# Kernel tuning notes

Measured on AMD Instinct MI355X. Metric: run time of the kernel, lower is better.

Reference implementation:

```python
import jax, jax.numpy as jnp
import numpy as np

B, S, D = 4, 1024, 4096
HQ, HKV, HD = 32, 8, 128
N_REP = HQ // HKV


def _rope(x, cos, sin):
    # x: [b, s, h, hd]; cos/sin: [s, hd//2]; pairs are (x[..., 2i], x[..., 2i+1])
    xr = x[..., 0::2]
    xi = x[..., 1::2]
    c = cos[None, :, None, :]
    s = sin[None, :, None, :]
    out_r = xr * c - xi * s
    out_i = xr * s + xi * c
    return jnp.stack([out_r, out_i], axis=-1).reshape(x.shape)


def setup_inputs() -> dict:
    key = jax.random.key(0)
    ks = jax.random.split(key, 6)
    x = jax.random.normal(ks[0], (B, S, D), dtype=jnp.float32)
    wq = jax.random.normal(ks[1], (HQ * HD, D), dtype=jnp.float32) * 0.02
    wk = jax.random.normal(ks[2], (HKV * HD, D), dtype=jnp.float32) * 0.02
    wv = jax.random.normal(ks[3], (HKV * HD, D), dtype=jnp.float32) * 0.02
    wo = jax.random.normal(ks[4], (D, HQ * HD), dtype=jnp.float32) * 0.02
    # standard rotary frequencies, theta=10000
    inv_freq = 1.0 / (10000.0 ** (np.arange(0, HD, 2, dtype=np.float32) / HD))
    angles = np.outer(np.arange(S, dtype=np.float32), inv_freq)  # [S, HD//2]
    freqs_cos = jnp.asarray(np.cos(angles), dtype=jnp.float32)
    freqs_sin = jnp.asarray(np.sin(angles), dtype=jnp.float32)
    cache_k = jnp.zeros((B, S, HKV, HD), dtype=jnp.float32)
    cache_v = jnp.zeros((B, S, HKV, HD), dtype=jnp.float32)
    return {"x": x, "wq": wq, "wk": wk, "wv": wv, "wo": wo,
            "freqs_cos": freqs_cos, "freqs_sin": freqs_sin,
            "cache_k": cache_k, "cache_v": cache_v, "start_pos": 0}


def reference(x, wq, wk, wv, wo, freqs_cos, freqs_sin, cache_k, cache_v, start_pos):
    b, s, _ = x.shape
    xq = jnp.einsum('bsd,od->bso', x, wq).reshape(b, s, HQ, HD)
    xk = jnp.einsum('bsd,od->bso', x, wk).reshape(b, s, HKV, HD)
    xv = jnp.einsum('bsd,od->bso', x, wv).reshape(b, s, HKV, HD)
    xq = _rope(xq, freqs_cos, freqs_sin)
    xk = _rope(xk, freqs_cos, freqs_sin)
    # KV-cache append (intended semantics: store keys/values)
    cache_k = jax.lax.dynamic_update_slice(cache_k, xk, (0, start_pos, 0, 0))
    cache_v = jax.lax.dynamic_update_slice(cache_v, xv, (0, start_pos, 0, 0))
    keys = cache_k[:, :start_pos + s]      # [b, kv, HKV, HD]
    values = cache_v[:, :start_pos + s]
    # GQA repeat_kv -> [b, kv, HQ, HD]
    keys = jnp.repeat(keys, N_REP, axis=2)
    values = jnp.repeat(values, N_REP, axis=2)
    scores = jnp.einsum('bqhd,bkhd->bhqk', xq, keys) / jnp.sqrt(jnp.float32(HD))
    probs = jax.nn.softmax(scores.astype(jnp.float32), axis=-1).astype(xq.dtype)
    out = jnp.einsum('bhqk,bkhd->bqhd', probs, values).reshape(b, s, HQ * HD)
    return jnp.einsum('bso,do->bsd', out, wo)
```

## Files before the change

### kernel.cpp

```cpp
#include <hip/hip_runtime.h>

typedef __bf16 bf16_t;
typedef __bf16 bf16x8 __attribute__((ext_vector_type(8)));
typedef __bf16 bf16x4 __attribute__((ext_vector_type(4)));
typedef float  f32x4  __attribute__((ext_vector_type(4)));
typedef short  s16x4  __attribute__((ext_vector_type(4)));

#define SEQ    1024
#define DMODEL 4096
#define NHQ    32
#define NHKV   8
#define HDIM   128

#define GLOAD_LDS16(g, l)                                                  \
    __builtin_amdgcn_global_load_lds(                                      \
        (const __attribute__((address_space(1))) unsigned int*)(g),        \
        (__attribute__((address_space(3))) unsigned int*)(l), 16, 0, 0)

__global__ __launch_bounds__(256)
void f2b(const float* __restrict__ in, bf16_t* __restrict__ out, int n8)
{
    int i = blockIdx.x * 256 + threadIdx.x;
    if (i >= n8) return;
    const float4* p = (const float4*)in + 2 * (size_t)i;
    float4 a = p[0], b = p[1];
    bf16x8 o;
    o[0] = (bf16_t)a.x; o[1] = (bf16_t)a.y; o[2] = (bf16_t)a.z; o[3] = (bf16_t)a.w;
    o[4] = (bf16_t)b.x; o[5] = (bf16_t)b.y; o[6] = (bf16_t)b.z; o[7] = (bf16_t)b.w;
    *((bf16x8*)out + i) = o;
}

#define MFMA_(a, b, c) __builtin_amdgcn_mfma_f32_16x16x32_bf16(a, b, c, 0, 0, 0)
#define BAR    __builtin_amdgcn_s_barrier()
#define SCB    __builtin_amdgcn_sched_barrier(0)
#define PRIO1  __builtin_amdgcn_s_setprio(1)
#define PRIO0  __builtin_amdgcn_s_setprio(0)
#define WLG0   do { asm volatile("s_waitcnt lgkmcnt(0)" ::: "memory"); SCB; } while (0)
#define WLG8   do { asm volatile("s_waitcnt lgkmcnt(8)" ::: "memory"); SCB; } while (0)
#define WVM4   do { asm volatile("s_waitcnt vmcnt(4)" ::: "memory"); SCB; } while (0)

#define SA(bufo, half, ktb)  do {                                          \
    const char* g_ = ((half) ? aS1 : aS0) + (ktb);                         \
    GLOAD_LDS16(g_,      sd + (bufo) + (half) * 8192);                     \
    GLOAD_LDS16(g_ + 64, sd + (bufo) + (half) * 8192 + 16384);             \
} while (0)
#define SB(bufo, half, ktb)  do {                                          \
    const char* g_ = ((half) ? bS1 : bS0) + (ktb);                         \
    GLOAD_LDS16(g_,      sd + (bufo) + 32768 + (half) * 8192);             \
    GLOAD_LDS16(g_ + 64, sd + (bufo) + 32768 + (half) * 8192 + 16384);     \
} while (0)
#define LDA(bufo, mh) do { _Pragma("unroll")                               \
    for (int j = 0; j < 4; ++j) {                                          \
        afq[j][0] = *(const bf16x8*)(lds + (bufo) + aRow + (mh)*4096 + j*1024);         \
        afq[j][1] = *(const bf16x8*)(lds + (bufo) + aRow + (mh)*4096 + j*1024 + 16384); \
    } } while (0)
#define LDB(bufo, nh, dst) do { _Pragma("unroll")                          \
    for (int n2 = 0; n2 < 2; ++n2) {                                       \
        dst[n2][0] = *(const bf16x8*)(lds + (bufo) + bRow + (nh)*2048 + n2*1024);         \
        dst[n2][1] = *(const bf16x8*)(lds + (bufo) + bRow + (nh)*2048 + n2*1024 + 16384); \
    } } while (0)
#define MMQ(mlo, bfx, nlo) do { _Pragma("unroll")                          \
    for (int j = 0; j < 4; ++j) {                                          \
        acc[(mlo)+j][(nlo)  ] = MFMA_(afq[j][0], bfx[0][0], acc[(mlo)+j][(nlo)  ]); \
        acc[(mlo)+j][(nlo)  ] = MFMA_(afq[j][1], bfx[0][1], acc[(mlo)+j][(nlo)  ]); \
        acc[(mlo)+j][(nlo)+1] = MFMA_(afq[j][0], bfx[1][0], acc[(mlo)+j][(nlo)+1]); \
        acc[(mlo)+j][(nlo)+1] = MFMA_(afq[j][1], bfx[1][1], acc[(mlo)+j][(nlo)+1]); \
    } } while (0)

template<bool OUT_F32>
__global__ __launch_bounds__(512, 2)
void gemm256(const bf16_t* __restrict__ A, const bf16_t* __restrict__ B,
             void* __restrict__ Cv, int M, int N, int K, int nbn)
{
    __shared__ __align__(16) char lds[131072];

    const int nwg = gridDim.x;
    const int bid0 = blockIdx.x;
    const int bid = (bid0 & 7) * (nwg >> 3) + (bid0 >> 3);
    const int bm = bid / nbn, bn = bid % nbn;
    const int t = threadIdx.x;
    const int lane = t & 63, wid = t >> 6;
    const int wm = wid >> 2, wn = wid & 3;
    const int l15 = lane & 15, lg = lane >> 4;
    const int m0 = bm * 256, n0 = bn * 256;

    const int Krb = K * 2;
    const int srow = t >> 2;
    const int schunk = (((t & 3) ^ ((t >> 3) & 3)) << 4);
    const char* aS0 = (const char*)A + (size_t)(m0 + srow) * Krb + schunk;
    const char* aS1 = (const char*)A + (size_t)(m0 + 128 + srow) * Krb + schunk;
    const char* bS0 = (const char*)B + (size_t)(n0 + srow) * Krb + schunk;
    const char* bS1 = (const char*)B + (size_t)(n0 + 128 + srow) * Krb + schunk;
    char* sd = lds + t * 16;

    const int rchunk = ((lg ^ ((l15 >> 1) & 3)) << 4);
    const int aRow = (wm * 128 + l15) * 64 + rchunk;
    const int bRow = 32768 + (wn * 64 + l15) * 64 + rchunk;

    const int NT = K >> 6;
    f32x4 acc[8][4] = {};
    bf16x8 afq[4][2], bf0[2][2], bf1[2][2];

    SA(0, 0, 0); SA(0, 1, 0); SB(0, 0, 0); SB(0, 1, 0);
    SB(65536, 0, 128); SB(65536, 1, 128);
    WVM4;
    BAR;

    for (int T = 0; T < NT; T += 2) {
        const int k1 = (T + 1) * 128;
        const int k2 = (T + 2 < NT) ? (T + 2) * 128 : 0;
        const int k3 = (T + 3 < NT) ? (T + 3) * 128 : 0;
        LDA(0, 0); LDB(0, 0, bf0); SA(65536, 0, k1); WLG8; BAR; WLG0;
        PRIO1; MMQ(0, bf0, 0); PRIO0; BAR;
        LDB(0, 1, bf1); SA(65536, 1, k1); BAR; WLG0;
        PRIO1; MMQ(0, bf1, 2); PRIO0; BAR;
        LDA(0, 1); SB(0, 0, k2); BAR; WLG0;
        PRIO1; MMQ(4, bf1, 2); PRIO0; BAR;
        SB(0, 1, k2); BAR;
        PRIO1; MMQ(4, bf0, 0); PRIO0; WVM4; BAR;
        LDA(65536, 0); LDB(65536, 0, bf0); SA(0, 0, k2); WLG8; BAR; WLG0;
        PRIO1; MMQ(0, bf0, 0); PRIO0; BAR;
        LDB(65536, 1, bf1); SA(0, 1, k2); BAR; WLG0;
        PRIO1; MMQ(0, bf1, 2); PRIO0; BAR;
        LDA(65536, 1); SB(65536, 0, k3); BAR; WLG0;
        PRIO1; MMQ(4, bf1, 2); PRIO0; BAR;
        SB(65536, 1, k3); BAR;
        PRIO1; MMQ(4, bf0, 0); PRIO0; WVM4; BAR;
    }

    #pragma unroll
    for (int m = 0; m < 8; ++m) {
        int row0 = m0 + wm * 128 + m * 16 + lg * 4;
        #pragma unroll
        for (int n = 0; n < 4; ++n) {
            int col = n0 + wn * 64 + n * 16 + l15;
            #pragma unroll
            for (int i = 0; i < 4; ++i) {
                if constexpr (OUT_F32)
                    ((float*)Cv)[(size_t)(row0 + i) * N + col] = acc[m][n][i];
                else
                    ((bf16_t*)Cv)[(size_t)(row0 + i) * N + col] = (bf16_t)acc[m][n][i];
            }
        }
    }
}

template<int MODE>
__global__ __launch_bounds__(256, 4)
void gemm_bt(const bf16_t* __restrict__ A, const bf16_t* __restrict__ B,
             void* __restrict__ Cv, bf16_t* __restrict__ Vt,
             int M, int N, int K, int nbn)
{
    __shared__ __align__(16) bf16_t lA[128 * 32];
    __shared__ __align__(16) bf16_t lB[128 * 32];

    const int nwg = gridDim.x;
    const int bid0 = blockIdx.x;
    const int bid = (bid0 & 7) * (nwg >> 3) + (bid0 >> 3);
    const int bm = bid / nbn, bn = bid % nbn;
    const int t = threadIdx.x;
    const int lane = t & 63, wid = t >> 6;
    const int wrow = (wid >> 1) * 64, wcol = (wid & 1) * 64;
    const int l15 = lane & 15, lg = lane >> 4;
    const int m0 = bm * 128, n0 = bn * 128;

    const int r0 = t >> 2, pos0 = (t & 3) * 8;
    const int r1 = r0 + 64;

    const bf16_t* Ar0 = A + (size_t)(m0 + r0) * K + pos0;
    const bf16_t* Ar1 = A + (size_t)(m0 + r1) * K + pos0;
    const bf16_t* Br0 = B + (size_t)(n0 + r0) * K + pos0;
    const bf16_t* Br1 = B + (size_t)(n0 + r1) * K + pos0;

    f32x4 acc[4][4] = {};

    for (int k0 = 0; k0 < K; k0 += 32) {
        __syncthreads();
        GLOAD_LDS16(Ar0 + k0, lA + t * 8);
        GLOAD_LDS16(Ar1 + k0, lA + (t + 256) * 8);
        GLOAD_LDS16(Br0 + k0, lB + t * 8);
        GLOAD_LDS16(Br1 + k0, lB + (t + 256) * 8);
        __syncthreads();

        bf16x8 af[4], bfr[4];
        #pragma unroll
        for (int m = 0; m < 4; ++m)
            af[m] = *(const bf16x8*)(lA + (wrow + m * 16 + l15) * 32 + lg * 8);
        #pragma unroll
        for (int n = 0; n < 4; ++n)
            bfr[n] = *(const bf16x8*)(lB + (wcol + n * 16 + l15) * 32 + lg * 8);
        #pragma unroll
        for (int m = 0; m < 4; ++m)
            #pragma unroll
            for (int n = 0; n < 4; ++n)
                acc[m][n] = __builtin_amdgcn_mfma_f32_16x16x32_bf16(
                    af[m], bfr[n], acc[m][n], 0, 0, 0);
    }

    #pragma unroll
    for (int m = 0; m < 4; ++m) {
        #pragma unroll
        for (int n = 0; n < 4; ++n) {
            int col  = n0 + wcol + n * 16 + l15;
            int row0 = m0 + wrow + m * 16 + lg * 4;
            if constexpr (MODE == 0) {
                #pragma unroll
                for (int i = 0; i < 4; ++i)
                    ((bf16_t*)Cv)[(size_t)(row0 + i) * N + col] = (bf16_t)acc[m][n][i];
            } else if constexpr (MODE == 1) {
                #pragma unroll
                for (int i = 0; i < 4; ++i)
                    ((float*)Cv)[(size_t)(row0 + i) * N + col] = acc[m][n][i];
            } else {
                if (col < 1024) {
                    #pragma unroll
                    for (int i = 0; i < 4; ++i)
                        ((bf16_t*)Cv)[(size_t)(row0 + i) * 1024 + col] = (bf16_t)acc[m][n][i];
                } else {
                    bf16x4 pk;
                    #pragma unroll
                    for (int i = 0; i < 4; ++i) pk[i] = (bf16_t)acc[m][n][i];
                    *(bf16x4*)(Vt + (size_t)(col - 1024) * 4096 + row0) = pk;
                }
            }
        }
    }
}

__global__ __launch_bounds__(256)
void rope_kernel(bf16_t* __restrict__ X, const float* __restrict__ fc,
                 const float* __restrict__ fs, int nheads, int rowstride)
{
    int idx = blockIdx.x * 256 + threadIdx.x;
    int j4 = idx & 15;
    int rest = idx >> 4;
    int h = rest % nheads;
    int tok = rest / nheads;
    int s = tok & (SEQ - 1);
    bf16_t* p = X + (size_t)tok * rowstride + h * HDIM + j4 * 8;
    bf16x8 v = *(const bf16x8*)p;
    float4 c  = *(const float4*)(fc + s * 64 + j4 * 4);
    float4 sn = *(const float4*)(fs + s * 64 + j4 * 4);
    bf16x8 o;
    o[0] = (bf16_t)((float)v[0] * c.x - (float)v[1] * sn.x);
    o[1] = (bf16_t)((float)v[0] * sn.x + (float)v[1] * c.x);
    o[2] = (bf16_t)((float)v[2] * c.y - (float)v[3] * sn.y);
    o[3] = (bf16_t)((float)v[2] * sn.y + (float)v[3] * c.y);
    o[4] = (bf16_t)((float)v[4] * c.z - (float)v[5] * sn.z);
    o[5] = (bf16_t)((float)v[4] * sn.z + (float)v[5] * c.z);
    o[6] = (bf16_t)((float)v[6] * c.w - (float)v[7] * sn.w);
    o[7] = (bf16_t)((float)v[6] * sn.w + (float)v[7] * c.w);
    *(bf16x8*)p = o;
}

__global__ __launch_bounds__(256, 4)
void attn_kernel(const bf16_t* __restrict__ Q, const bf16_t* __restrict__ Kg,
                 const bf16_t* __restrict__ Vtg, bf16_t* __restrict__ O)
{
    __shared__ __align__(16) char klds[64 * 256];
    __shared__ __align__(16) char vlds[128 * 128];

    const int nwg = gridDim.x;
    const int bid0 = blockIdx.x;
    const int blk = (bid0 & 7) * (nwg >> 3) + (bid0 >> 3);
    const int qt = blk & 15;
    const int bh = blk >> 4;
    const int b = bh >> 5, h = bh & 31, kv = h >> 2;
    const int t = threadIdx.x, lane = t & 63, wid = t >> 6;
    const int l15 = lane & 15, lg = lane >> 4;
    const int swzk = (l15 & 7) << 4;

    const float SCL = 0.08838834764831845f;
    const float L2E = 1.4426950408889634f;

    const int qrow = qt * 64 + wid * 16 + l15;
    const size_t qbase = (size_t)(b * SEQ + qrow) * DMODEL + h * HDIM;
    bf16x8 qf[4];
    #pragma unroll
    for (int dc = 0; dc < 4; ++dc)
        qf[dc] = *(const bf16x8*)(Q + qbase + dc * 32 + lg * 8);

    const char* kgb = (const char*)Kg + ((size_t)(b * SEQ) * 1024 + kv * HDIM) * 2;
    const char* vgb = (const char*)Vtg + ((size_t)(kv * HDIM) * 4096 + b * SEQ) * 2;

    f32x4 o[8] = {};
    float mrun = -3.0e38f, lrun = 0.f;

    for (int kt = 0; kt < 16; ++kt) {
        __syncthreads();
        #pragma unroll
        for (int i = 0; i < 4; ++i) {
            int idx = t + 256 * i;
            {
                int r = idx >> 4, cb = (idx & 15) << 4;
                const char* src = kgb + (size_t)(kt * 64 + r) * 2048
                                      + (cb ^ ((r & 7) << 4));
                GLOAD_LDS16(src, klds + idx * 16);
            }
            {
                int d = idx >> 3, cb = (idx & 7) << 4;
                const char* src = vgb + (size_t)d * 8192 + kt * 128
                                      + (cb ^ ((d & 7) << 4));
                GLOAD_LDS16(src, vlds + idx * 16);
            }
        }
        __syncthreads();

        f32x4 sacc[4] = {};
        #pragma unroll
        for (int kb = 0; kb < 4; ++kb) {
            const char* krow = klds + (kb * 16 + l15) * 256;
            #pragma unroll
            for (int dc = 0; dc < 4; ++dc) {
                bf16x8 kf = *(const bf16x8*)(krow + ((dc * 64 + lg * 16) ^ swzk));
                sacc[kb] = __builtin_amdgcn_mfma_f32_16x16x32_bf16(
                    kf, qf[dc], sacc[kb], 0, 0, 0);
            }
        }

        float sv[16];
        float mt = -3.0e38f;
        #pragma unroll
        for (int kb = 0; kb < 4; ++kb)
            #pragma unroll
            for (int i = 0; i < 4; ++i) {
                float s = sacc[kb][i] * SCL;
                sv[kb * 4 + i] = s;
                mt = fmaxf(mt, s);
            }
        mt = fmaxf(mt, __shfl_xor(mt, 16));
        mt = fmaxf(mt, __shfl_xor(mt, 32));
        float mnew = fmaxf(mrun, mt);
        float alpha = exp2f((mrun - mnew) * L2E);

        float ts = 0.f;
        s16x4 pf[4];
        #pragma unroll
        for (int kb = 0; kb < 4; ++kb)
            #pragma unroll
            for (int i = 0; i < 4; ++i) {
                float p = exp2f((sv[kb * 4 + i] - mnew) * L2E);
                ts += p;
                pf[kb][i] = (short)__builtin_bit_cast(unsigned short, (bf16_t)p);
            }
        ts += __shfl_xor(ts, 16);
        ts += __shfl_xor(ts, 32);
        lrun = lrun * alpha + ts;
        mrun = mnew;

        #pragma unroll
        for (int i = 0; i < 4; ++i) {
            float ai = __shfl(alpha, lg * 4 + i);
            #pragma unroll
            for (int db = 0; db < 8; ++db) o[db][i] *= ai;
        }

        #pragma unroll
        for (int kb = 0; kb < 4; ++kb)
            #pragma unroll
            for (int db = 0; db < 8; ++db) {
                int d = l15 + 16 * db;
                const char* va = vlds + d * 128 + ((kb * 32 + lg * 8) ^ swzk);
                s16x4 vf = *(const s16x4*)va;
                o[db] = __builtin_amdgcn_mfma_f32_16x16x16bf16_1k(
                    pf[kb], vf, o[db], 0, 0, 0);
            }
    }

    #pragma unroll
    for (int i = 0; i < 4; ++i) {
        float li = __shfl(lrun, lg * 4 + i);
        float inv = 1.0f / li;
        int row = b * SEQ + qt * 64 + wid * 16 + lg * 4 + i;
        #pragma unroll
        for (int db = 0; db < 8; ++db) {
            int col = h * HDIM + l15 + 16 * db;
            O[(size_t)row * DMODEL + col] = (bf16_t)(o[db][i] * inv);
        }
    }
}

extern "C" void kernel_launch(void* const* d_in, const int* in_sizes, int n_in,
                              void* d_out, int out_size, void* d_ws, size_t ws_size,
                              hipStream_t stream)
{
    const float* x  = (const float*)d_in[0];
    const float* wq = (const float*)d_in[1];
    const float* wk = (const float*)d_in[2];
    const float* wv = (const float*)d_in[3];
    const float* wo = (const float*)d_in[4];
    const float* fc = (const float*)d_in[5];
    const float* fs = (const float*)d_in[6];

    const size_t T = (size_t)4096;
    bf16_t* Qw   = (bf16_t*)d_ws;
    bf16_t* Kw2  = Qw   + T * 4096;
    bf16_t* Vt   = Kw2  + T * 1024;
    bf16_t* AO   = Vt   + T * 1024;
    bf16_t* xb   = AO   + T * 4096;
    bf16_t* wqb  = xb   + T * 4096;
    bf16_t* wkvb = wqb  + T * 4096;
    bf16_t* wob  = wkvb + T * 2048;

    f2b<<<8192, 256, 0, stream>>>(x,  xb,  4096 * 4096 / 8);
    f2b<<<8192, 256, 0, stream>>>(wq, wqb, 4096 * 4096 / 8);
    f2b<<<2048, 256, 0, stream>>>(wk, wkvb,                       1024 * 4096 / 8);
    f2b<<<2048, 256, 0, stream>>>(wv, wkvb + (size_t)1024 * 4096, 1024 * 4096 / 8);
    f2b<<<8192, 256, 0, stream>>>(wo, wob, 4096 * 4096 / 8);

    gemm256<false><<<256, 512, 0, stream>>>(xb, wqb, Qw, 4096, 4096, 4096, 16);
    gemm_bt<2><<<512, 256, 0, stream>>>(xb, wkvb, Kw2, Vt, 4096, 2048, 4096, 16);

    rope_kernel<<<8192, 256, 0, stream>>>(Qw,  fc, fs, NHQ,  4096);
    rope_kernel<<<2048, 256, 0, stream>>>(Kw2, fc, fs, NHKV, 1024);

    attn_kernel<<<2048, 256, 0, stream>>>(Qw, Kw2, Vt, AO);

    gemm256<true><<<256, 512, 0, stream>>>(AO, wob, d_out, 4096, 4096, 4096, 16);
}
```

Baseline: 526.9 us.

## Double-buffer KV tiles in attention, widen to 128-row Q tiles, fold scale into RoPE

The attention kernel now uses 512-thread blocks covering 128 query rows, so each K/V tile loaded into LDS serves twice as many queries. K/V tiles are double-buffered, with the next tile's loads issued before computing on the current one, leaving one barrier per iteration. The 1/sqrt(d) softmax scale moves into the Q RoPE pass, which removes a multiply per score. LDS use doubles and occupancy changes to 2 blocks of 512 threads, and the grid halves to 1024 blocks.

```diff
diff --git a/kernel.cpp b/kernel.cpp
--- a/kernel.cpp
+++ b/kernel.cpp
@@ -229,7 +229,8 @@
 
 __global__ __launch_bounds__(256)
 void rope_kernel(bf16_t* __restrict__ X, const float* __restrict__ fc,
-                 const float* __restrict__ fs, int nheads, int rowstride)
+                 const float* __restrict__ fs, int nheads, int rowstride,
+                 float oscale)
 {
     int idx = blockIdx.x * 256 + threadIdx.x;
     int j4 = idx & 15;
@@ -241,6 +242,8 @@
     bf16x8 v = *(const bf16x8*)p;
     float4 c  = *(const float4*)(fc + s * 64 + j4 * 4);
     float4 sn = *(const float4*)(fs + s * 64 + j4 * 4);
+    c.x *= oscale; c.y *= oscale; c.z *= oscale; c.w *= oscale;
+    sn.x *= oscale; sn.y *= oscale; sn.z *= oscale; sn.w *= oscale;
     bf16x8 o;
     o[0] = (bf16_t)((float)v[0] * c.x - (float)v[1] * sn.x);
     o[1] = (bf16_t)((float)v[0] * sn.x + (float)v[1] * c.x);
@@ -253,27 +256,26 @@
     *(bf16x8*)p = o;
 }
 
-__global__ __launch_bounds__(256, 4)
+__global__ __launch_bounds__(512, 2)
 void attn_kernel(const bf16_t* __restrict__ Q, const bf16_t* __restrict__ Kg,
                  const bf16_t* __restrict__ Vtg, bf16_t* __restrict__ O)
 {
-    __shared__ __align__(16) char klds[64 * 256];
-    __shared__ __align__(16) char vlds[128 * 128];
+    __shared__ __align__(16) char klds[2][64 * 256];
+    __shared__ __align__(16) char vlds[2][128 * 128];
 
     const int nwg = gridDim.x;
     const int bid0 = blockIdx.x;
     const int blk = (bid0 & 7) * (nwg >> 3) + (bid0 >> 3);
-    const int qt = blk & 15;
-    const int bh = blk >> 4;
+    const int qt = blk & 7;
+    const int bh = blk >> 3;
     const int b = bh >> 5, h = bh & 31, kv = h >> 2;
     const int t = threadIdx.x, lane = t & 63, wid = t >> 6;
     const int l15 = lane & 15, lg = lane >> 4;
     const int swzk = (l15 & 7) << 4;
 
-    const float SCL = 0.08838834764831845f;
     const float L2E = 1.4426950408889634f;
 
-    const int qrow = qt * 64 + wid * 16 + l15;
+    const int qrow = qt * 128 + wid * 16 + l15;
     const size_t qbase = (size_t)(b * SEQ + qrow) * DMODEL + h * HDIM;
     bf16x8 qf[4];
     #pragma unroll
@@ -283,33 +285,34 @@
     const char* kgb = (const char*)Kg + ((size_t)(b * SEQ) * 1024 + kv * HDIM) * 2;
     const char* vgb = (const char*)Vtg + ((size_t)(kv * HDIM) * 4096 + b * SEQ) * 2;
 
+    const int ck0 = t, ck1 = t + 512;
+    const int kr0 = ck0 >> 4, kf0 = kr0 * 2048 + ((((ck0 & 15) << 4)) ^ ((kr0 & 7) << 4));
+    const int kr1 = ck1 >> 4, kf1 = kr1 * 2048 + ((((ck1 & 15) << 4)) ^ ((kr1 & 7) << 4));
+    const int vd0 = ck0 >> 3, vf0 = vd0 * 8192 + ((((ck0 & 7) << 4)) ^ ((vd0 & 7) << 4));
+    const int vd1 = ck1 >> 3, vf1 = vd1 * 8192 + ((((ck1 & 7) << 4)) ^ ((vd1 & 7) << 4));
+
     f32x4 o[8] = {};
     float mrun = -3.0e38f, lrun = 0.f;
 
+#define STAGE_KV(kt_, bi_) do {                                            \
+    GLOAD_LDS16(kgb + (size_t)(kt_) * 131072 + kf0, klds[bi_] + ck0 * 16); \
+    GLOAD_LDS16(kgb + (size_t)(kt_) * 131072 + kf1, klds[bi_] + ck1 * 16); \
+    GLOAD_LDS16(vgb + (kt_) * 128 + vf0, vlds[bi_] + ck0 * 16);            \
+    GLOAD_LDS16(vgb + (kt_) * 128 + vf1, vlds[bi_] + ck1 * 16);            \
+} while (0)
+
+    STAGE_KV(0, 0);
+    __syncthreads();
+
     for (int kt = 0; kt < 16; ++kt) {
-        __syncthreads();
-        #pragma unroll
-        for (int i = 0; i < 4; ++i) {
-            int idx = t + 256 * i;
-            {
-                int r = idx >> 4, cb = (idx & 15) << 4;
-                const char* src = kgb + (size_t)(kt * 64 + r) * 2048
-                                      + (cb ^ ((r & 7) << 4));
-                GLOAD_LDS16(src, klds + idx * 16);
-            }
-            {
-                int d = idx >> 3, cb = (idx & 7) << 4;
-                const char* src = vgb + (size_t)d * 8192 + kt * 128
-                                      + (cb ^ ((d & 7) << 4));
-                GLOAD_LDS16(src, vlds + idx * 16);
-            }
-        }
-        __syncthreads();
+        const int cur = kt & 1;
+        const int knx = (kt + 1 < 16) ? kt + 1 : 15;
+        STAGE_KV(knx, cur ^ 1);
 
         f32x4 sacc[4] = {};
         #pragma unroll
         for (int kb = 0; kb < 4; ++kb) {
-            const char* krow = klds + (kb * 16 + l15) * 256;
+            const char* krow = klds[cur] + (kb * 16 + l15) * 256;
             #pragma unroll
             for (int dc = 0; dc < 4; ++dc) {
                 bf16x8 kf = *(const bf16x8*)(krow + ((dc * 64 + lg * 16) ^ swzk));
@@ -324,7 +327,7 @@
         for (int kb = 0; kb < 4; ++kb)
             #pragma unroll
             for (int i = 0; i < 4; ++i) {
-                float s = sacc[kb][i] * SCL;
+                float s = sacc[kb][i];
                 sv[kb * 4 + i] = s;
                 mt = fmaxf(mt, s);
             }
@@ -360,18 +363,21 @@
             #pragma unroll
             for (int db = 0; db < 8; ++db) {
                 int d = l15 + 16 * db;
-                const char* va = vlds + d * 128 + ((kb * 32 + lg * 8) ^ swzk);
+                const char* va = vlds[cur] + d * 128 + ((kb * 32 + lg * 8) ^ swzk);
                 s16x4 vf = *(const s16x4*)va;
                 o[db] = __builtin_amdgcn_mfma_f32_16x16x16bf16_1k(
                     pf[kb], vf, o[db], 0, 0, 0);
             }
-    }
+
+        __syncthreads();
+    }
+#undef STAGE_KV
 
     #pragma unroll
     for (int i = 0; i < 4; ++i) {
         float li = __shfl(lrun, lg * 4 + i);
         float inv = 1.0f / li;
-        int row = b * SEQ + qt * 64 + wid * 16 + lg * 4 + i;
+        int row = b * SEQ + qt * 128 + wid * 16 + lg * 4 + i;
         #pragma unroll
         for (int db = 0; db < 8; ++db) {
             int col = h * HDIM + l15 + 16 * db;
@@ -411,10 +417,11 @@
     gemm256<false><<<256, 512, 0, stream>>>(xb, wqb, Qw, 4096, 4096, 4096, 16);
     gemm_bt<2><<<512, 256, 0, stream>>>(xb, wkvb, Kw2, Vt, 4096, 2048, 4096, 16);
 
-    rope_kernel<<<8192, 256, 0, stream>>>(Qw,  fc, fs, NHQ,  4096);
-    rope_kernel<<<2048, 256, 0, stream>>>(Kw2, fc, fs, NHKV, 1024);
-
-    attn_kernel<<<2048, 256, 0, stream>>>(Qw, Kw2, Vt, AO);
+    rope_kernel<<<8192, 256, 0, stream>>>(Qw,  fc, fs, NHQ,  4096,
+                                          0.08838834764831845f);
+    rope_kernel<<<2048, 256, 0, stream>>>(Kw2, fc, fs, NHKV, 1024, 1.0f);
+
+    attn_kernel<<<1024, 512, 0, stream>>>(Qw, Kw2, Vt, AO);
 
     gemm256<true><<<256, 512, 0, stream>>>(AO, wob, d_out, 4096, 4096, 4096, 16);
 }
```

Result: no change. 519.3 us (-1.4%).
